# Optimization experiments

Hardware: AMD Instinct MI355X
Metric: run time of the kernel (lower is better)

The kernel has to match this reference:

```python
import jax, jax.numpy as jnp
import numpy as np

EPS = 1e-6
ROPE_THETA = 10000.0
NUM_HEADS = 32
NUM_KV_HEADS = 8
HEAD_DIM = 128
HIDDEN = 4096
B, S = 2, 2048


def setup_inputs() -> dict:
    key = jax.random.key(0)
    ks = jax.random.split(key, 6)
    scale = 0.02
    return {
        "hidden_states": jax.random.normal(ks[0], (B, S, HIDDEN), dtype=jnp.float32),
        "position_ids": jnp.arange(S, dtype=jnp.int64 if jax.config.jax_enable_x64 else jnp.int32)[None, :],
        "Wq": jax.random.normal(ks[1], (HIDDEN, NUM_HEADS * HEAD_DIM), dtype=jnp.float32) * scale,
        "Wk": jax.random.normal(ks[2], (HIDDEN, NUM_KV_HEADS * HEAD_DIM), dtype=jnp.float32) * scale,
        "Wv": jax.random.normal(ks[3], (HIDDEN, NUM_KV_HEADS * HEAD_DIM), dtype=jnp.float32) * scale,
        "Wo": jax.random.normal(ks[4], (NUM_HEADS * HEAD_DIM, HIDDEN), dtype=jnp.float32) * scale,
        "q_norm_w": jnp.ones((HEAD_DIM,), dtype=jnp.float32),
        "k_norm_w": jnp.ones((HEAD_DIM,), dtype=jnp.float32),
    }


def _rms_norm(x, w):
    # RMSNorm over last dim (head_dim)
    var = jnp.mean(jnp.square(x), axis=-1, keepdims=True)
    return x * jax.lax.rsqrt(var + EPS) * w


def _rope(x, position_ids):
    # x: [B, H, S, D]; Llama-style half-split rotation
    d = x.shape[-1]
    inv_freq = 1.0 / (ROPE_THETA ** (jnp.arange(0, d, 2, dtype=jnp.float32) / d))  # [D/2]
    ang = position_ids[:, :, None].astype(jnp.float32) * inv_freq[None, None, :]   # [B, S, D/2]
    emb = jnp.concatenate([ang, ang], axis=-1)                                     # [B, S, D]
    cos = jnp.cos(emb)[:, None, :, :]
    sin = jnp.sin(emb)[:, None, :, :]
    x1, x2 = x[..., : d // 2], x[..., d // 2:]
    rot = jnp.concatenate([-x2, x1], axis=-1)
    return x * cos + rot * sin


def reference(hidden_states, position_ids, Wq, Wk, Wv, Wo, q_norm_w, k_norm_w):
    b, s, _ = hidden_states.shape
    q = (hidden_states @ Wq).reshape(b, s, NUM_HEADS, HEAD_DIM).transpose(0, 2, 1, 3)
    k = (hidden_states @ Wk).reshape(b, s, NUM_KV_HEADS, HEAD_DIM).transpose(0, 2, 1, 3)
    v = (hidden_states @ Wv).reshape(b, s, NUM_KV_HEADS, HEAD_DIM).transpose(0, 2, 1, 3)

    q = _rms_norm(q, q_norm_w)
    k = _rms_norm(k, k_norm_w)

    q = _rope(q, position_ids)
    k = _rope(k, position_ids)

    groups = NUM_HEADS // NUM_KV_HEADS
    k = jnp.repeat(k, groups, axis=1)  # repeat_interleave along head dim
    v = jnp.repeat(v, groups, axis=1)

    scale = 1.0 / jnp.sqrt(jnp.float32(HEAD_DIM))
    scores = jnp.einsum("bhqd,bhkd->bhqk", q, k) * scale
    causal = jnp.tril(jnp.ones((s, s), dtype=bool))
    scores = jnp.where(causal[None, None], scores, jnp.finfo(scores.dtype).min)
    attn = jax.nn.softmax(scores, axis=-1)
    out = jnp.einsum("bhqk,bhkd->bhqd", attn, v)
    out = out.transpose(0, 2, 1, 3).reshape(b, s, NUM_HEADS * HEAD_DIM)
    return out @ Wo
```

## Files before the change

kernel.cpp:

```cpp
#include <hip/hip_runtime.h>
#include <stdint.h>
#include <stddef.h>

#define S_LEN 2048
#define BATCH 2
#define NHEADS 32
#define NKV 8
#define HD 128
#define HIDDEN 4096
#define T_TOK (BATCH * S_LEN)
#define QKV_W 6144

typedef unsigned short u16;
typedef __attribute__((ext_vector_type(4))) float f32x4;
typedef __attribute__((ext_vector_type(16))) float f32x16;
typedef __attribute__((ext_vector_type(8))) short s16x8;
typedef __attribute__((ext_vector_type(4))) unsigned short u16x4;
typedef __attribute__((ext_vector_type(4))) unsigned int u32x4;

__device__ __forceinline__ u16 f2bf(float f) {
  unsigned int u = __builtin_bit_cast(unsigned int, f);
  unsigned int r = (u + 0x7FFFu + ((u >> 16) & 1u)) >> 16;
  return (u16)r;
}
__device__ __forceinline__ float bf2f(u16 h) {
  return __builtin_bit_cast(float, ((unsigned int)h) << 16);
}

__device__ __forceinline__ void gload16(const void* g, void* l) {
  __builtin_amdgcn_global_load_lds((__attribute__((address_space(1))) void*)g,
                                   (__attribute__((address_space(3))) void*)l,
                                   16, 0, 0);
}

__device__ __forceinline__ unsigned cvtpk(float a, float b) {
  unsigned r;
  asm("v_cvt_pk_bf16_f32 %0, %1, %2" : "=v"(r) : "v"(a), "v"(b));
  return r;
}
__device__ __forceinline__ void lohi_dup(unsigned W, unsigned& lo, unsigned& hi) {
  unsigned a = W, b = W;
  asm volatile("v_permlane32_swap_b32 %0, %1" : "+v"(a), "+v"(b));
  lo = a; hi = b;
}

__global__ __launch_bounds__(256) void k_convert(const float* __restrict__ in,
                                                 u16* __restrict__ out, int n8) {
  int i = blockIdx.x * 256 + threadIdx.x;
  if (i >= n8) return;
  float4 a = ((const float4*)in)[i * 2];
  float4 b = ((const float4*)in)[i * 2 + 1];
  u16x4 lo = {f2bf(a.x), f2bf(a.y), f2bf(a.z), f2bf(a.w)};
  u16x4 hi = {f2bf(b.x), f2bf(b.y), f2bf(b.z), f2bf(b.w)};
  ((u16x4*)out)[i * 2] = lo;
  ((u16x4*)out)[i * 2 + 1] = hi;
}

__global__ __launch_bounds__(256) void k_transpose_w(const float* __restrict__ W,
                                                     u16* __restrict__ Wt, int K,
                                                     int N, int outRowOff,
                                                     int outStride) {
  __shared__ float tl[32][33];
  int k0 = blockIdx.x * 32, n0 = blockIdx.y * 32;
  int t = threadIdx.x;
  int r = t >> 3, c4 = (t & 7) * 4;
  float4 v = *(const float4*)&W[(size_t)(k0 + r) * N + n0 + c4];
  tl[r][c4] = v.x; tl[r][c4 + 1] = v.y; tl[r][c4 + 2] = v.z; tl[r][c4 + 3] = v.w;
  __syncthreads();
  u16x4 o = {f2bf(tl[c4][r]), f2bf(tl[c4 + 1][r]), f2bf(tl[c4 + 2][r]),
             f2bf(tl[c4 + 3][r])};
  *(u16x4*)&Wt[(size_t)(outRowOff + n0 + r) * outStride + k0 + c4] = o;
}

__global__ __launch_bounds__(256) void k_rope_tab(const int* __restrict__ pos,
                                                  float* __restrict__ tab) {
  int i = blockIdx.x * 256 + threadIdx.x;
  int s = i >> 6, l = i & 63;
  float p = (float)pos[s];
  float ang = p * expf(-(float)l * 0.14391156516342163f);
  tab[s * 128 + l] = cosf(ang);
  tab[s * 128 + 64 + l] = sinf(ang);
}

template <typename OutT>
__global__ __launch_bounds__(512, 2) void k_gemm256(const u16* __restrict__ A,
                                                    const u16* __restrict__ Bt,
                                                    OutT* __restrict__ C,
                                                    int N, int K) {
  __shared__ u16 As[2][16384];
  __shared__ u16 Bs[2][16384];
  int nbn = N >> 8;
  int nwg = gridDim.x;
  int orig = blockIdx.x;
  int q8 = nwg >> 3, r8 = nwg & 7;
  int xcd = orig & 7, sub = orig >> 3;
  int wgid = (xcd < r8 ? xcd * (q8 + 1) : r8 * (q8 + 1) + (xcd - r8) * q8) + sub;
  int bm = wgid / nbn, bn = wgid % nbn;
  int tid = threadIdx.x, wid = tid >> 6, lane = tid & 63;
  int wm = wid >> 2, wn = wid & 3;
  int g = lane >> 4, c = lane & 15;
  int l3 = lane >> 3, l7 = lane & 7;
  int swz = c & 7;
  int xunit = (l7 ^ l3) * 8;

  f32x4 acc[8][4];
#pragma unroll
  for (int m = 0; m < 8; m++)
#pragma unroll
    for (int n = 0; n < 4; n++) acc[m][n] = (f32x4){0.f, 0.f, 0.f, 0.f};

  const u16* aBase = A + (size_t)(bm * 256 + wid * 16 + l3) * K + xunit;
  const u16* bBase = Bt + (size_t)(bn * 256 + wid * 16 + l3) * K + xunit;

  auto stgA = [&](int buf, int h, int j, size_t koff) {
    gload16(aBase + (size_t)(h * 128 + j * 8) * K + koff,
            &As[buf][(h * 128 + wid * 16 + j * 8) * 64]);
  };
  auto stgB = [&](int buf, int h, int j, size_t koff) {
    gload16(bBase + (size_t)(h * 128 + j * 8) * K + koff,
            &Bs[buf][(h * 128 + wid * 16 + j * 8) * 64]);
  };

  int nt = K >> 6;
#pragma unroll
  for (int j = 0; j < 2; j++) {
    stgA(0, 0, j, 0); stgA(0, 1, j, 0);
    stgB(0, 0, j, 0); stgB(0, 1, j, 0);
  }
#pragma unroll
  for (int j = 0; j < 2; j++) { stgB(1, 0, j, 64); stgB(1, 1, j, 64); }
  asm volatile("s_waitcnt vmcnt(4)" ::: "memory");
  __builtin_amdgcn_s_barrier();

  for (int t = 0; t < nt; t++) {
    int cb = t & 1;
    const u16* Ab = &As[cb][0];
    const u16* Bb = &Bs[cb][0];
    size_t k1 = (size_t)(t + 1) << 6;
    size_t k2 = (size_t)(t + 2) << 6;
    bool s1 = (t + 1 < nt), s2 = (t + 2 < nt);
    s16x8 af[8], bf0[4], bf1[4];

#pragma unroll
    for (int mi = 0; mi < 4; mi++)
#pragma unroll
      for (int ks = 0; ks < 2; ks++)
        af[mi * 2 + ks] = *(const s16x8*)&Ab[(wm * 128 + mi * 16 + c) * 64 +
                                             (((ks * 4 + g) ^ swz) * 8)];
#pragma unroll
    for (int nj = 0; nj < 2; nj++)
#pragma unroll
      for (int ks = 0; ks < 2; ks++)
        bf0[nj * 2 + ks] = *(const s16x8*)&Bb[(wn * 64 + nj * 16 + c) * 64 +
                                              (((ks * 4 + g) ^ swz) * 8)];
    if (s1) { stgA(cb ^ 1, 0, 0, k1); stgA(cb ^ 1, 0, 1, k1); }
    __builtin_amdgcn_s_barrier();
    asm volatile("s_waitcnt lgkmcnt(0)" ::: "memory");
    __builtin_amdgcn_sched_barrier(0);
    __builtin_amdgcn_s_setprio(1);
#pragma unroll
    for (int mi = 0; mi < 4; mi++)
#pragma unroll
      for (int nj = 0; nj < 2; nj++)
#pragma unroll
        for (int ks = 0; ks < 2; ks++)
          acc[mi][nj] = __builtin_amdgcn_mfma_f32_16x16x32_bf16(
              af[mi * 2 + ks], bf0[nj * 2 + ks], acc[mi][nj], 0, 0, 0);
    __builtin_amdgcn_s_setprio(0);
    __builtin_amdgcn_s_barrier();

#pragma unroll
    for (int nj = 0; nj < 2; nj++)
#pragma unroll
      for (int ks = 0; ks < 2; ks++)
        bf1[nj * 2 + ks] = *(const s16x8*)&Bb[(wn * 64 + (2 + nj) * 16 + c) * 64 +
                                              (((ks * 4 + g) ^ swz) * 8)];
    if (s1) { stgA(cb ^ 1, 1, 0, k1); stgA(cb ^ 1, 1, 1, k1); }
    __builtin_amdgcn_s_barrier();
    asm volatile("s_waitcnt lgkmcnt(0)" ::: "memory");
    __builtin_amdgcn_sched_barrier(0);
    __builtin_amdgcn_s_setprio(1);
#pragma unroll
    for (int mi = 0; mi < 4; mi++)
#pragma unroll
      for (int nj = 0; nj < 2; nj++)
#pragma unroll
        for (int ks = 0; ks < 2; ks++)
          acc[mi][2 + nj] = __builtin_amdgcn_mfma_f32_16x16x32_bf16(
              af[mi * 2 + ks], bf1[nj * 2 + ks], acc[mi][2 + nj], 0, 0, 0);
    __builtin_amdgcn_s_setprio(0);
    __builtin_amdgcn_s_barrier();

#pragma unroll
    for (int mi = 0; mi < 4; mi++)
#pragma unroll
      for (int ks = 0; ks < 2; ks++)
        af[mi * 2 + ks] = *(const s16x8*)&Ab[(wm * 128 + 64 + mi * 16 + c) * 64 +
                                             (((ks * 4 + g) ^ swz) * 8)];
    if (s2) { stgB(cb, 0, 0, k2); stgB(cb, 0, 1, k2); }
    __builtin_amdgcn_s_barrier();
    asm volatile("s_waitcnt lgkmcnt(0)" ::: "memory");
    __builtin_amdgcn_sched_barrier(0);
    __builtin_amdgcn_s_setprio(1);
#pragma unroll
    for (int mi = 0; mi < 4; mi++)
#pragma unroll
      for (int nj = 0; nj < 2; nj++)
#pragma unroll
        for (int ks = 0; ks < 2; ks++)
          acc[4 + mi][nj] = __builtin_amdgcn_mfma_f32_16x16x32_bf16(
              af[mi * 2 + ks], bf0[nj * 2 + ks], acc[4 + mi][nj], 0, 0, 0);
    __builtin_amdgcn_s_setprio(0);
    __builtin_amdgcn_s_barrier();

    if (s2) { stgB(cb, 1, 0, k2); stgB(cb, 1, 1, k2); }
    __builtin_amdgcn_s_setprio(1);
#pragma unroll
    for (int mi = 0; mi < 4; mi++)
#pragma unroll
      for (int nj = 0; nj < 2; nj++)
#pragma unroll
        for (int ks = 0; ks < 2; ks++)
          acc[4 + mi][2 + nj] = __builtin_amdgcn_mfma_f32_16x16x32_bf16(
              af[mi * 2 + ks], bf1[nj * 2 + ks], acc[4 + mi][2 + nj], 0, 0, 0);
    __builtin_amdgcn_s_setprio(0);
    if (s2)
      asm volatile("s_waitcnt vmcnt(4)" ::: "memory");
    else if (s1)
      asm volatile("s_waitcnt vmcnt(0)" ::: "memory");
    __builtin_amdgcn_s_barrier();
  }

#pragma unroll
  for (int m = 0; m < 8; m++)
#pragma unroll
    for (int n = 0; n < 4; n++) {
      size_t row = (size_t)bm * 256 + wm * 128 + m * 16 + g * 4;
      size_t col = (size_t)bn * 256 + wn * 64 + n * 16 + c;
#pragma unroll
      for (int r = 0; r < 4; r++) {
        float v = acc[m][n][r];
        if constexpr (sizeof(OutT) == 2)
          C[(row + r) * N + col] = (OutT)f2bf(v);
        else
          C[(row + r) * N + col] = (OutT)v;
      }
    }
}

__global__ __launch_bounds__(256) void k_rmsrope(u16* __restrict__ QK,
                                                 const float* __restrict__ w,
                                                 const float* __restrict__ tab,
                                                 int H, int rowStride) {
  int row = blockIdx.x * 4 + (threadIdx.x >> 6);
  int lane = threadIdx.x & 63;
  int t = row / H, h = row - t * H;
  int s = t & (S_LEN - 1);
  u16* p = QK + (size_t)t * rowStride + h * HD;
  float x1 = bf2f(p[lane]), x2 = bf2f(p[lane + 64]);
  float ss = x1 * x1 + x2 * x2;
#pragma unroll
  for (int o = 32; o >= 1; o >>= 1) ss += __shfl_xor(ss, o);
  float inv = rsqrtf(ss * (1.0f / 128.0f) + 1e-6f);
  float y1 = x1 * inv * w[lane], y2 = x2 * inv * w[lane + 64];
  float cs = tab[s * 128 + lane], sn = tab[s * 128 + 64 + lane];
  p[lane] = f2bf(y1 * cs - y2 * sn);
  p[lane + 64] = f2bf(y2 * cs + y1 * sn);
}

__global__ __launch_bounds__(256) void k_transpose_v(const u16* __restrict__ QKV,
                                                     u16* __restrict__ Vt) {
  __shared__ u16 tl[32][40];
  int bkh = blockIdx.x;
  int s0 = blockIdx.y * 32, d0 = blockIdx.z * 32;
  int b = bkh >> 3, kh = bkh & 7;
  int t = threadIdx.x, r = t >> 3, c4 = (t & 7) * 4;
  const u16* src =
      QKV + (size_t)(b * S_LEN + s0 + r) * QKV_W + 5120 + kh * HD + d0 + c4;
  u16x4 v = *(const u16x4*)src;
  tl[r][c4] = v[0]; tl[r][c4 + 1] = v[1]; tl[r][c4 + 2] = v[2]; tl[r][c4 + 3] = v[3];
  __syncthreads();
  u16x4 o = {tl[c4][r], tl[c4 + 1][r], tl[c4 + 2][r], tl[c4 + 3][r]};
  *(u16x4*)&Vt[(size_t)(bkh * HD + d0 + r) * S_LEN + s0 + c4] = o;
}

__global__ __launch_bounds__(256) void k_attn(const u16* __restrict__ QKV,
                                              const u16* __restrict__ Vt,
                                              u16* __restrict__ Oact) {
  __shared__ u16 Ks[2][64 * 128];
  __shared__ u16 Vs[2][128 * 64];
  int bid = blockIdx.x;
  int xcd = bid & 7, slot = bid >> 3;
  int grp = xcd * 2 + (slot >> 5);
  int b = grp >> 3, kh = grp & 7;
  int s32 = slot & 31;
  int pr = s32 >> 2;
  int h = kh * 4 + (s32 & 3);
  int w = threadIdx.x >> 6, lane = threadIdx.x & 63;
  int q31 = lane & 31, hh = lane >> 5;
  const float qscale = 0.12751740810f;

  const char* Kg = (const char*)(QKV + (size_t)b * S_LEN * QKV_W + 4096 + kh * HD);
  const char* Vg = (const char*)(Vt + (size_t)(b * 8 + kh) * HD * S_LEN);

#pragma unroll 1
  for (int half = 0; half < 2; half++) {
    __syncthreads();
    int qt = half ? 15 - pr : pr;
    int qw0 = qt * 128 + w * 32;

    s16x8 qf[8];
    const u16* Qp = QKV + (size_t)(b * S_LEN + qw0 + q31) * QKV_W + h * HD + hh * 8;
#pragma unroll
    for (int dc = 0; dc < 8; dc++) {
      s16x8 raw = *(const s16x8*)(Qp + dc * 16);
#pragma unroll
      for (int e = 0; e < 8; e++)
        qf[dc][e] = (short)f2bf(bf2f((u16)raw[e]) * qscale);
    }

    f32x16 o[4];
#pragma unroll
    for (int d = 0; d < 4; d++)
#pragma unroll
      for (int r = 0; r < 16; r++) o[d][r] = 0.f;
    float m = -3.0e38f, l = 0.f;

    int nch = 2 * qt + 2;

    {
      char* KsB = (char*)Ks[0];
      char* VsB = (char*)Vs[0];
#pragma unroll
      for (int j = 0; j < 4; j++) {
        int ins = w * 4 + j;
        int row = ins * 4 + (lane >> 4);
        int bc = ((lane & 15) * 16) ^ ((row & 7) << 4);
        gload16(Kg + (size_t)row * 12288 + bc, KsB + ins * 1024);
      }
#pragma unroll
      for (int j = 0; j < 4; j++) {
        int ins = w * 4 + j;
        int row = ins * 8 + (lane >> 3);
        int bc = ((lane & 7) * 16) ^ ((row & 7) << 4);
        gload16(Vg + (size_t)row * 4096 + bc, VsB + ins * 1024);
      }
    }

    int cur = 0;
    for (int ch = 0; ch < nch; ch++) {
      int kb = ch * 64;
      __syncthreads();
      if (ch + 1 < nch) {
        char* KsB = (char*)Ks[cur ^ 1];
        char* VsB = (char*)Vs[cur ^ 1];
        int kb2 = kb + 64;
#pragma unroll
        for (int j = 0; j < 4; j++) {
          int ins = w * 4 + j;
          int row = ins * 4 + (lane >> 4);
          int bc = ((lane & 15) * 16) ^ ((row & 7) << 4);
          gload16(Kg + (size_t)(kb2 + row) * 12288 + bc, KsB + ins * 1024);
        }
#pragma unroll
        for (int j = 0; j < 4; j++) {
          int ins = w * 4 + j;
          int row = ins * 8 + (lane >> 3);
          int bc = ((lane & 7) * 16) ^ ((row & 7) << 4);
          gload16(Vg + (size_t)row * 4096 + (size_t)kb2 * 2 + bc, VsB + ins * 1024);
        }
      }
      if (kb <= qw0 + 31) {
        char* KsB = (char*)Ks[cur];
        char* VsB = (char*)Vs[cur];
        f32x16 sA, sB;
#pragma unroll
        for (int r = 0; r < 16; r++) { sA[r] = 0.f; sB[r] = 0.f; }
        int sw = (q31 & 7) << 4;
        __builtin_amdgcn_s_setprio(1);
#pragma unroll
        for (int dc = 0; dc < 8; dc++) {
          s16x8 kfA = *(const s16x8*)(KsB + q31 * 256 + ((dc * 32 + hh * 16) ^ sw));
          s16x8 kfB = *(const s16x8*)(KsB + (32 + q31) * 256 + ((dc * 32 + hh * 16) ^ sw));
          sA = __builtin_amdgcn_mfma_f32_32x32x16_bf16(kfA, qf[dc], sA, 0, 0, 0);
          sB = __builtin_amdgcn_mfma_f32_32x32x16_bf16(kfB, qf[dc], sB, 0, 0, 0);
        }
        __builtin_amdgcn_s_setprio(0);
        if (kb + 63 > qw0) {
          int qa = qw0 + q31;
#pragma unroll
          for (int r = 0; r < 16; r++) {
            int krow = (r & 3) + 8 * (r >> 2) + 4 * hh;
            if (kb + krow > qa) sA[r] = -1e30f;
            if (kb + 32 + krow > qa) sB[r] = -1e30f;
          }
        }
        float mx = -3.0e38f;
#pragma unroll
        for (int r = 0; r < 16; r++) mx = fmaxf(mx, fmaxf(sA[r], sB[r]));
        mx = fmaxf(mx, __shfl_xor(mx, 32));
        if (!__all(mx - m <= 11.5f)) {
          float mnew = fmaxf(m, mx);
          float corr = __builtin_amdgcn_exp2f(m - mnew);
          l *= corr;
#pragma unroll
          for (int d = 0; d < 4; d++)
#pragma unroll
            for (int r = 0; r < 16; r++) o[d][r] *= corr;
          m = mnew;
        }
        float rs = 0.f;
#pragma unroll
        for (int r = 0; r < 16; r++) {
          sA[r] = __builtin_amdgcn_exp2f(sA[r] - m); rs += sA[r];
          sB[r] = __builtin_amdgcn_exp2f(sB[r] - m); rs += sB[r];
        }
        rs += __shfl_xor(rs, 32);
        l += rs;
#pragma unroll
        for (int st = 0; st < 2; st++) {
          unsigned Aw[8], Bw[8];
#pragma unroll
          for (int j = 0; j < 8; j++) {
            float p0 = st ? sB[2 * j] : sA[2 * j];
            float p1 = st ? sB[2 * j + 1] : sA[2 * j + 1];
            lohi_dup(cvtpk(p0, p1), Aw[j], Bw[j]);
          }
#pragma unroll
          for (int kc2 = 0; kc2 < 2; kc2++) {
            u32x4 wv;
            wv.x = hh ? Aw[kc2 * 4 + 2] : Aw[kc2 * 4 + 0];
            wv.y = hh ? Aw[kc2 * 4 + 3] : Aw[kc2 * 4 + 1];
            wv.z = hh ? Bw[kc2 * 4 + 2] : Bw[kc2 * 4 + 0];
            wv.w = hh ? Bw[kc2 * 4 + 3] : Bw[kc2 * 4 + 1];
            s16x8 pf = __builtin_bit_cast(s16x8, wv);
            int kc = st * 2 + kc2;
            __builtin_amdgcn_s_setprio(1);
#pragma unroll
            for (int d = 0; d < 4; d++) {
              int row = d * 32 + q31;
              int vsw = (row & 7) << 4;
              s16x8 vf = *(const s16x8*)(VsB + row * 128 + ((kc * 32 + hh * 16) ^ vsw));
              o[d] = __builtin_amdgcn_mfma_f32_32x32x16_bf16(vf, pf, o[d], 0, 0, 0);
            }
            __builtin_amdgcn_s_setprio(0);
          }
        }
      }
      cur ^= 1;
    }
    float linv = 1.0f / l;
    u16* Op = Oact + (size_t)(b * S_LEN + qw0 + q31) * 4096 + h * HD;
#pragma unroll
    for (int d = 0; d < 4; d++)
#pragma unroll
      for (int g4 = 0; g4 < 4; g4++) {
        int d0 = d * 32 + 8 * g4 + 4 * hh;
        u16x4 w4 = {f2bf(o[d][4 * g4 + 0] * linv), f2bf(o[d][4 * g4 + 1] * linv),
                    f2bf(o[d][4 * g4 + 2] * linv), f2bf(o[d][4 * g4 + 3] * linv)};
        *(u16x4*)(Op + d0) = w4;
      }
  }
}

extern "C" void kernel_launch(void* const* d_in, const int* in_sizes, int n_in,
                              void* d_out, int out_size, void* d_ws,
                              size_t ws_size, hipStream_t stream) {
  (void)in_sizes; (void)n_in; (void)out_size; (void)ws_size;
  const float* X = (const float*)d_in[0];
  const int* pos = (const int*)d_in[1];
  const float* Wq = (const float*)d_in[2];
  const float* Wk = (const float*)d_in[3];
  const float* Wv = (const float*)d_in[4];
  const float* Wo = (const float*)d_in[5];
  const float* qw = (const float*)d_in[6];
  const float* kw = (const float*)d_in[7];
  float* out = (float*)d_out;
  char* ws = (char*)d_ws;

  const size_t MB = 1024ull * 1024ull;
  u16* Xb    = (u16*)(ws + 0 * MB);
  u16* WqkvT = (u16*)(ws + 32 * MB);
  u16* WkvT  = (u16*)(ws + 64 * MB);
  u16* WoT   = (u16*)(ws + 80 * MB);
  u16* QKV   = (u16*)(ws + 112 * MB);
  u16* Vt    = (u16*)(ws + 160 * MB);
  u16* Oact  = (u16*)(ws + 168 * MB);
  float* tab = (float*)(ws + 200 * MB);

  k_convert<<<8192, 256, 0, stream>>>(X, Xb, (T_TOK * HIDDEN) / 8);
  k_transpose_w<<<dim3(128, 128), 256, 0, stream>>>(Wq, WqkvT, 4096, 4096, 0, 4096);
  k_transpose_w<<<dim3(128, 32), 256, 0, stream>>>(Wk, WkvT, 4096, 1024, 0, 4096);
  k_transpose_w<<<dim3(128, 32), 256, 0, stream>>>(Wv, WkvT, 4096, 1024, 1024, 4096);
  k_transpose_w<<<dim3(128, 128), 256, 0, stream>>>(Wo, WoT, 4096, 4096, 0, 4096);
  k_rope_tab<<<512, 256, 0, stream>>>(pos, tab);

  k_gemm256<u16><<<16 * 24, 512, 0, stream>>>(Xb, WqkvT, QKV, QKV_W, 4096);

  k_rmsrope<<<(T_TOK * NHEADS) / 4, 256, 0, stream>>>(QKV, qw, tab, NHEADS, QKV_W);
  k_rmsrope<<<(T_TOK * NKV) / 4, 256, 0, stream>>>(QKV + 4096, kw, tab, NKV, QKV_W);

  k_transpose_v<<<dim3(16, 64, 4), 256, 0, stream>>>(QKV, Vt);

  k_attn<<<512, 256, 0, stream>>>(QKV, Vt, Oact);

  k_gemm256<float><<<16 * 16, 512, 0, stream>>>(Oact, WoT, out, 4096, 4096);
}
```

Before: 636.1 us.

## Replace 256x256 pipelined GEMM with simpler 128x128 tile GEMM

Shrinks the GEMM workgroup tile from 256x256 with 512 threads to 128x128 with 256 threads, using a straightforward double-buffered loop with one barrier per K step. The finer tiles raise the block count to reduce wave-quantization tail on the QKV and output projections. In exchange it lowers data reuse per tile and drops the fine-grained interleaving of loads, barriers and MFMA phases, so memory latency may be less well hidden.

```diff
diff --git a/kernel.cpp b/kernel.cpp
--- a/kernel.cpp
+++ b/kernel.cpp
@@ -83,13 +83,13 @@
 }
 
 template <typename OutT>
-__global__ __launch_bounds__(512, 2) void k_gemm256(const u16* __restrict__ A,
+__global__ __launch_bounds__(256, 2) void k_gemm128(const u16* __restrict__ A,
                                                     const u16* __restrict__ Bt,
                                                     OutT* __restrict__ C,
                                                     int N, int K) {
-  __shared__ u16 As[2][16384];
-  __shared__ u16 Bs[2][16384];
-  int nbn = N >> 8;
+  __shared__ u16 As[2][8192];
+  __shared__ u16 Bs[2][8192];
+  int nbn = N >> 7;
   int nwg = gridDim.x;
   int orig = blockIdx.x;
   int q8 = nwg >> 3, r8 = nwg & 7;
@@ -97,146 +97,76 @@
   int wgid = (xcd < r8 ? xcd * (q8 + 1) : r8 * (q8 + 1) + (xcd - r8) * q8) + sub;
   int bm = wgid / nbn, bn = wgid % nbn;
   int tid = threadIdx.x, wid = tid >> 6, lane = tid & 63;
-  int wm = wid >> 2, wn = wid & 3;
+  int wm = wid >> 1, wn = wid & 1;
   int g = lane >> 4, c = lane & 15;
   int l3 = lane >> 3, l7 = lane & 7;
   int swz = c & 7;
   int xunit = (l7 ^ l3) * 8;
 
-  f32x4 acc[8][4];
-#pragma unroll
-  for (int m = 0; m < 8; m++)
+  f32x4 acc[4][4];
+#pragma unroll
+  for (int m = 0; m < 4; m++)
 #pragma unroll
     for (int n = 0; n < 4; n++) acc[m][n] = (f32x4){0.f, 0.f, 0.f, 0.f};
 
-  const u16* aBase = A + (size_t)(bm * 256 + wid * 16 + l3) * K + xunit;
-  const u16* bBase = Bt + (size_t)(bn * 256 + wid * 16 + l3) * K + xunit;
-
-  auto stgA = [&](int buf, int h, int j, size_t koff) {
-    gload16(aBase + (size_t)(h * 128 + j * 8) * K + koff,
-            &As[buf][(h * 128 + wid * 16 + j * 8) * 64]);
+  const u16* aBase = A + (size_t)(bm * 128 + wid * 32 + l3) * K + xunit;
+  const u16* bBase = Bt + (size_t)(bn * 128 + wid * 32 + l3) * K + xunit;
+
+  auto stgA = [&](int buf, int j, size_t koff) {
+    gload16(aBase + (size_t)(j * 8) * K + koff, &As[buf][(wid * 32 + j * 8) * 64]);
   };
-  auto stgB = [&](int buf, int h, int j, size_t koff) {
-    gload16(bBase + (size_t)(h * 128 + j * 8) * K + koff,
-            &Bs[buf][(h * 128 + wid * 16 + j * 8) * 64]);
+  auto stgB = [&](int buf, int j, size_t koff) {
+    gload16(bBase + (size_t)(j * 8) * K + koff, &Bs[buf][(wid * 32 + j * 8) * 64]);
   };
 
   int nt = K >> 6;
 #pragma unroll
-  for (int j = 0; j < 2; j++) {
-    stgA(0, 0, j, 0); stgA(0, 1, j, 0);
-    stgB(0, 0, j, 0); stgB(0, 1, j, 0);
-  }
-#pragma unroll
-  for (int j = 0; j < 2; j++) { stgB(1, 0, j, 64); stgB(1, 1, j, 64); }
-  asm volatile("s_waitcnt vmcnt(4)" ::: "memory");
-  __builtin_amdgcn_s_barrier();
+  for (int j = 0; j < 4; j++) { stgA(0, j, 0); stgB(0, j, 0); }
+  __syncthreads();
 
   for (int t = 0; t < nt; t++) {
     int cb = t & 1;
     const u16* Ab = &As[cb][0];
     const u16* Bb = &Bs[cb][0];
+    bool s1 = (t + 1 < nt);
     size_t k1 = (size_t)(t + 1) << 6;
-    size_t k2 = (size_t)(t + 2) << 6;
-    bool s1 = (t + 1 < nt), s2 = (t + 2 < nt);
-    s16x8 af[8], bf0[4], bf1[4];
-
+
+    s16x8 af[4][2], bf[4][2];
 #pragma unroll
     for (int mi = 0; mi < 4; mi++)
 #pragma unroll
       for (int ks = 0; ks < 2; ks++)
-        af[mi * 2 + ks] = *(const s16x8*)&Ab[(wm * 128 + mi * 16 + c) * 64 +
-                                             (((ks * 4 + g) ^ swz) * 8)];
-#pragma unroll
-    for (int nj = 0; nj < 2; nj++)
+        af[mi][ks] = *(const s16x8*)&Ab[(wm * 64 + mi * 16 + c) * 64 +
+                                        (((ks * 4 + g) ^ swz) * 8)];
+#pragma unroll
+    for (int nj = 0; nj < 4; nj++)
 #pragma unroll
       for (int ks = 0; ks < 2; ks++)
-        bf0[nj * 2 + ks] = *(const s16x8*)&Bb[(wn * 64 + nj * 16 + c) * 64 +
-                                              (((ks * 4 + g) ^ swz) * 8)];
-    if (s1) { stgA(cb ^ 1, 0, 0, k1); stgA(cb ^ 1, 0, 1, k1); }
-    __builtin_amdgcn_s_barrier();
-    asm volatile("s_waitcnt lgkmcnt(0)" ::: "memory");
-    __builtin_amdgcn_sched_barrier(0);
+        bf[nj][ks] = *(const s16x8*)&Bb[(wn * 64 + nj * 16 + c) * 64 +
+                                        (((ks * 4 + g) ^ swz) * 8)];
+    if (s1) {
+#pragma unroll
+      for (int j = 0; j < 4; j++) { stgA(cb ^ 1, j, k1); stgB(cb ^ 1, j, k1); }
+    }
     __builtin_amdgcn_s_setprio(1);
 #pragma unroll
     for (int mi = 0; mi < 4; mi++)
 #pragma unroll
-      for (int nj = 0; nj < 2; nj++)
+      for (int nj = 0; nj < 4; nj++)
 #pragma unroll
         for (int ks = 0; ks < 2; ks++)
           acc[mi][nj] = __builtin_amdgcn_mfma_f32_16x16x32_bf16(
-              af[mi * 2 + ks], bf0[nj * 2 + ks], acc[mi][nj], 0, 0, 0);
+              af[mi][ks], bf[nj][ks], acc[mi][nj], 0, 0, 0);
     __builtin_amdgcn_s_setprio(0);
-    __builtin_amdgcn_s_barrier();
-
-#pragma unroll
-    for (int nj = 0; nj < 2; nj++)
-#pragma unroll
-      for (int ks = 0; ks < 2; ks++)
-        bf1[nj * 2 + ks] = *(const s16x8*)&Bb[(wn * 64 + (2 + nj) * 16 + c) * 64 +
-                                              (((ks * 4 + g) ^ swz) * 8)];
-    if (s1) { stgA(cb ^ 1, 1, 0, k1); stgA(cb ^ 1, 1, 1, k1); }
-    __builtin_amdgcn_s_barrier();
-    asm volatile("s_waitcnt lgkmcnt(0)" ::: "memory");
-    __builtin_amdgcn_sched_barrier(0);
-    __builtin_amdgcn_s_setprio(1);
-#pragma unroll
-    for (int mi = 0; mi < 4; mi++)
-#pragma unroll
-      for (int nj = 0; nj < 2; nj++)
-#pragma unroll
-        for (int ks = 0; ks < 2; ks++)
-          acc[mi][2 + nj] = __builtin_amdgcn_mfma_f32_16x16x32_bf16(
-              af[mi * 2 + ks], bf1[nj * 2 + ks], acc[mi][2 + nj], 0, 0, 0);
-    __builtin_amdgcn_s_setprio(0);
-    __builtin_amdgcn_s_barrier();
-
-#pragma unroll
-    for (int mi = 0; mi < 4; mi++)
-#pragma unroll
-      for (int ks = 0; ks < 2; ks++)
-        af[mi * 2 + ks] = *(const s16x8*)&Ab[(wm * 128 + 64 + mi * 16 + c) * 64 +
-                                             (((ks * 4 + g) ^ swz) * 8)];
-    if (s2) { stgB(cb, 0, 0, k2); stgB(cb, 0, 1, k2); }
-    __builtin_amdgcn_s_barrier();
-    asm volatile("s_waitcnt lgkmcnt(0)" ::: "memory");
-    __builtin_amdgcn_sched_barrier(0);
-    __builtin_amdgcn_s_setprio(1);
-#pragma unroll
-    for (int mi = 0; mi < 4; mi++)
-#pragma unroll
-      for (int nj = 0; nj < 2; nj++)
-#pragma unroll
-        for (int ks = 0; ks < 2; ks++)
-          acc[4 + mi][nj] = __builtin_amdgcn_mfma_f32_16x16x32_bf16(
-              af[mi * 2 + ks], bf0[nj * 2 + ks], acc[4 + mi][nj], 0, 0, 0);
-    __builtin_amdgcn_s_setprio(0);
-    __builtin_amdgcn_s_barrier();
-
-    if (s2) { stgB(cb, 1, 0, k2); stgB(cb, 1, 1, k2); }
-    __builtin_amdgcn_s_setprio(1);
-#pragma unroll
-    for (int mi = 0; mi < 4; mi++)
-#pragma unroll
-      for (int nj = 0; nj < 2; nj++)
-#pragma unroll
-        for (int ks = 0; ks < 2; ks++)
-          acc[4 + mi][2 + nj] = __builtin_amdgcn_mfma_f32_16x16x32_bf16(
-              af[mi * 2 + ks], bf1[nj * 2 + ks], acc[4 + mi][2 + nj], 0, 0, 0);
-    __builtin_amdgcn_s_setprio(0);
-    if (s2)
-      asm volatile("s_waitcnt vmcnt(4)" ::: "memory");
-    else if (s1)
-      asm volatile("s_waitcnt vmcnt(0)" ::: "memory");
-    __builtin_amdgcn_s_barrier();
+    __syncthreads();
   }
 
 #pragma unroll
-  for (int m = 0; m < 8; m++)
+  for (int m = 0; m < 4; m++)
 #pragma unroll
     for (int n = 0; n < 4; n++) {
-      size_t row = (size_t)bm * 256 + wm * 128 + m * 16 + g * 4;
-      size_t col = (size_t)bn * 256 + wn * 64 + n * 16 + c;
+      size_t row = (size_t)bm * 128 + wm * 64 + m * 16 + g * 4;
+      size_t col = (size_t)bn * 128 + wn * 64 + n * 16 + c;
 #pragma unroll
       for (int r = 0; r < 4; r++) {
         float v = acc[m][n][r];
@@ -495,7 +425,7 @@
   k_transpose_w<<<dim3(128, 128), 256, 0, stream>>>(Wo, WoT, 4096, 4096, 0, 4096);
   k_rope_tab<<<512, 256, 0, stream>>>(pos, tab);
 
-  k_gemm256<u16><<<16 * 24, 512, 0, stream>>>(Xb, WqkvT, QKV, QKV_W, 4096);
+  k_gemm128<u16><<<32 * 48, 256, 0, stream>>>(Xb, WqkvT, QKV, QKV_W, 4096);
 
   k_rmsrope<<<(T_TOK * NHEADS) / 4, 256, 0, stream>>>(QKV, qw, tab, NHEADS, QKV_W);
   k_rmsrope<<<(T_TOK * NKV) / 4, 256, 0, stream>>>(QKV + 4096, kw, tab, NKV, QKV_W);
@@ -504,5 +434,5 @@
 
   k_attn<<<512, 256, 0, stream>>>(QKV, Vt, Oact);
 
-  k_gemm256<float><<<16 * 16, 512, 0, stream>>>(Oact, WoT, out, 4096, 4096);
-}
+  k_gemm128<float><<<32 * 32, 256, 0, stream>>>(Oact, WoT, out, 4096, 4096);
+}
```

New measurement: 658.8 us. +3.6%, slower.
